# Optimization experiments

Hardware: AMD Instinct MI355X
Metric: run time of the kernel (lower is better)

The kernel has to match this reference:

```python
import jax, jax.numpy as jnp
import numpy as np
from jax import lax

K = 3      # kernel_size
C = 64     # n_feat
B, H, W = 2, 256, 256


def _conv(x, w, b, pad):
    # NCHW conv, stride 1
    out = lax.conv_general_dilated(x, w, (1, 1), [(pad, pad), (pad, pad)],
                                   dimension_numbers=('NCHW', 'OIHW', 'NCHW'))
    return out + b[None, :, None, None]


def _prelu(x, a):
    # nn.PReLU() with a single shared learnable slope (init 0.25)
    return jnp.where(x >= 0, x, a * x)


def setup_inputs():
    key = jax.random.key(0)
    ks = jax.random.split(key, 20)
    s = 0.05
    def w(k, shape):
        return jax.random.normal(k, shape, jnp.float32) * s
    inp = {
        'image': jax.random.normal(ks[0], (B, C, H, W), jnp.float32),
        'guidance': jax.random.normal(ks[1], (B, C, H, W), jnp.float32),
        # self.tensor: 1x1 conv (2C -> C) + PReLU (shared with jbf_conv's act)
        'tensor_w': w(ks[2], (C, 2 * C, 1, 1)),
        'tensor_b': jnp.zeros((C,), jnp.float32),
        'a_jbf': jnp.full((1,), 0.25, jnp.float32),
        'kg_w1': w(ks[3], (C, C, 3, 3)), 'kg_b1': jnp.zeros((C,), jnp.float32),
        'kg_w2': w(ks[4], (C, C, 3, 3)), 'kg_b2': jnp.zeros((C,), jnp.float32),
        'kg_w3': w(ks[5], (C, C, 3, 3)), 'kg_b3': jnp.zeros((C,), jnp.float32),
        'kg_w4': w(ks[6], (C, C, 3, 3)), 'kg_b4': jnp.zeros((C,), jnp.float32),
        'kg_w5': w(ks[7], (K * K * C, C, 1, 1)),
        'kg_b5': jnp.zeros((K * K * C,), jnp.float32),
        'a_kg': jnp.full((1,), 0.25, jnp.float32),
        # jbf_conv: 3x3 C->C, PReLU (shared a_jbf), 3x3 C->C
        'jbf_w1': w(ks[8], (C, C, 3, 3)), 'jbf_b1': jnp.zeros((C,), jnp.float32),
        'jbf_w2': w(ks[9], (C, C, 3, 3)), 'jbf_b2': jnp.zeros((C,), jnp.float32),
    }
    return inp


def reference(image, guidance, tensor_w, tensor_b, a_jbf,
              kg_w1, kg_b1, kg_w2, kg_b2, kg_w3, kg_b3, kg_w4, kg_b4,
              kg_w5, kg_b5, a_kg, jbf_w1, jbf_b1, jbf_w2, jbf_b2):
    b, c, h, w = image.shape
    # fuse target+guidance features
    t = _prelu(_conv(jnp.concatenate([image, guidance], axis=1), tensor_w, tensor_b, 0), a_jbf)
    # concat_kg: predict per-pixel dynamic kernel (b, K*K*c, h, w)
    y = t
    for wt, bs in ((kg_w1, kg_b1), (kg_w2, kg_b2), (kg_w3, kg_b3), (kg_w4, kg_b4)):
        y = _prelu(_conv(y, wt, bs, 1), a_kg)
    bi_kernel = _conv(y, kg_w5, kg_b5, 0)
    # unfold: torch layout is channel-major (c, ki, kj) along dim 1
    p = (K - 1) // 2
    xp = jnp.pad(image, ((0, 0), (0, 0), (p, p), (p, p)))
    taps = [xp[:, :, i:i + h, j:j + w] for i in range(K) for j in range(K)]
    patch = jnp.stack(taps, axis=2).reshape(b, c * K * K, h, w)
    # NOTE: faithful to source -- (c*K*K) flat layout reinterpreted as (K*K, c)
    jbf = (patch * bi_kernel).reshape(b, K * K, c, h, w).sum(axis=1)
    out = _conv(_prelu(_conv(jbf, jbf_w1, jbf_b1, 1), a_jbf), jbf_w2, jbf_b2, 1)
    return out + image
```

## Files before the change

kernel.cpp:

```cpp
#include <hip/hip_runtime.h>

#define HW 65536

typedef __bf16 bf16x8 __attribute__((ext_vector_type(8)));
typedef float f32x16 __attribute__((ext_vector_type(16)));

__device__ inline unsigned short f2bf(float x) {
    union { float f; unsigned u; } v; v.f = x;
    unsigned r = v.u + 0x7FFF + ((v.u >> 16) & 1);
    return (unsigned short)(r >> 16);
}
__device__ inline float bfhi2f(unsigned u) {
    union { unsigned u; float f; } v; v.u = u & 0xffff0000u; return v.f;
}
__device__ inline float bflo2f(unsigned u) {
    union { unsigned u; float f; } v; v.u = u << 16; return v.f;
}

union FragU { uint4 u; bf16x8 v; };
__device__ inline bf16x8 ld_frag(const uint4* p) { FragU t; t.u = *p; return t.v; }


__global__ __launch_bounds__(256) void k_wprep(
    const float* __restrict__ w0, const float* __restrict__ w1,
    const float* __restrict__ w2, const float* __restrict__ w3,
    const float* __restrict__ w4, const float* __restrict__ w5,
    const float* __restrict__ w5c, const float* __restrict__ tw,
    unsigned short* __restrict__ wT)
{
    int y = blockIdx.y;
    unsigned short* o = wT + (size_t)y * 36864;
    if (y < 6) {
        const float* ws_[6] = {w0, w1, w2, w3, w4, w5};
        const float* w = ws_[y];
        for (int e = blockIdx.x * 256 + threadIdx.x; e < 36864; e += gridDim.x * 256) {
            int tap = e >> 12, oc = (e >> 6) & 63, ic = e & 63;
            int igg = ic >> 3, j = ic & 7;
            int dst = ((tap * 8 + igg) * 64 + oc) * 8 + j;
            o[dst] = f2bf(w[(oc * 64 + ic) * 9 + tap]);
        }
    } else if (y == 6) {
        for (int e = blockIdx.x * 256 + threadIdx.x; e < 36864; e += gridDim.x * 256)
            o[e] = f2bf(w5c[e]);
    } else {
        for (int e = blockIdx.x * 256 + threadIdx.x; e < 8192; e += gridDim.x * 256) {
            int oc = e >> 7, ic = e & 127;
            int kg = ic >> 3, j = ic & 7;
            o[((kg * 64 + oc) << 3) + j] = f2bf(tw[e]);
        }
    }
}

__global__ __launch_bounds__(256) void k_tr(
    const float* __restrict__ img, const float* __restrict__ gd,
    unsigned short* __restrict__ imgT, unsigned short* __restrict__ gdT)
{
    __shared__ float sT[64 * 66];
    int tid = threadIdx.x;
    int z = blockIdx.y;
    int b = z & 1;
    const float* src = (z >> 1) ? gd : img;
    unsigned short* dst = (z >> 1) ? gdT : imgT;
    int px0 = blockIdx.x * 64;
    size_t sbase = (size_t)b * 64 * HW + px0;

#pragma unroll
    for (int i = 0; i < 4; ++i) {
        int e = i * 256 + tid;
        int ic = e >> 4, seg = e & 15;
        float4 v = *(const float4*)(src + sbase + (size_t)ic * HW + seg * 4);
        float* p = &sT[ic * 66 + seg * 4];
        ((float2*)p)[0] = make_float2(v.x, v.y);
        ((float2*)p)[1] = make_float2(v.z, v.w);
    }
    __syncthreads();

    size_t dbase = (size_t)b * HW * 64 + (size_t)px0 * 64;
#pragma unroll
    for (int k = 0; k < 2; ++k) {
        int idx = k * 256 + tid;
        int px = idx >> 3, u = idx & 7;
        union { uint4 q; unsigned short h[8]; } o;
#pragma unroll
        for (int j = 0; j < 8; ++j)
            o.h[j] = f2bf(sT[(u * 8 + j) * 66 + px]);
        *(uint4*)(dst + dbase + (size_t)px * 64 + u * 8) = o.q;
    }
}

__global__ __launch_bounds__(256, 4) void k_fusem(
    const unsigned short* __restrict__ imgT, const unsigned short* __restrict__ gdT,
    const unsigned short* __restrict__ wTf, const float* __restrict__ bias,
    const float* __restrict__ a, unsigned short* __restrict__ out)
{
    __shared__ __align__(16) char smem[18688];
    uint4* sX = (uint4*)smem;
    float* sB = (float*)(smem + 18432);
    unsigned short* sT16 = (unsigned short*)smem;

    int tid = threadIdx.x;
    int wv = tid >> 6, lane = tid & 63;
    int half = lane >> 5, l31 = lane & 31;
    int lin = blockIdx.x + (blockIdx.y << 4) + (blockIdx.z << 9);
    int slab = lin & 7, sub = lin >> 3;
    int b = slab >> 2;
    int y0 = (slab & 3) * 64 + (sub >> 4) * 8;
    int x0 = (sub & 15) * 16;
    size_t zbase = (size_t)b * HW * 64;
    const uint4* wg = (const uint4*)wTf;

    if (tid < 64) sB[tid] = bias[tid];

    f32x16 acc[2];
#pragma unroll
    for (int i = 0; i < 2; ++i)
#pragma unroll
        for (int r = 0; r < 16; ++r) acc[i][r] = 0.f;

    auto loadX = [&](const unsigned short* src, uint4* rx) {
#pragma unroll
        for (int i = 0; i < 4; ++i) {
            int e = i * 256 + tid;
            int px = e >> 3, ig = e & 7;
            int gy = y0 + (px >> 4), gx = x0 + (px & 15);
            rx[i] = *(const uint4*)(src + zbase + ((size_t)(gy * 256 + gx)) * 64 + ig * 8);
        }
    };
    auto writeX = [&](const uint4* rx) {
#pragma unroll
        for (int i = 0; i < 4; ++i) {
            int e = i * 256 + tid;
            sX[(e >> 3) * 9 + (e & 7)] = rx[i];
        }
    };
    auto compute = [&](int h) {
#pragma unroll
        for (int c = 0; c < 4; ++c) {
            int ig = c * 2 + half;
            int kg = h * 8 + ig;
            bf16x8 a0 = ld_frag(&wg[kg * 64 + l31]);
            bf16x8 a1 = ld_frag(&wg[kg * 64 + 32 + l31]);
            int p0 = wv * 32 + l31;
            bf16x8 b0 = ld_frag(&sX[p0 * 9 + ig]);
            acc[0] = __builtin_amdgcn_mfma_f32_32x32x16_bf16(a0, b0, acc[0], 0, 0, 0);
            acc[1] = __builtin_amdgcn_mfma_f32_32x32x16_bf16(a1, b0, acc[1], 0, 0, 0);
        }
    };

    uint4 rx[4], ry[4];
    loadX(imgT, rx);
    writeX(rx);
    loadX(gdT, ry);
    __syncthreads();
    compute(0);
    __syncthreads();
    writeX(ry);
    __syncthreads();
    compute(1);

    float slope = a[0];
    __syncthreads();
    {
        int px = wv * 32 + l31;
#pragma unroll
        for (int ot = 0; ot < 2; ++ot)
#pragma unroll
            for (int q2 = 0; q2 < 4; ++q2) {
                unsigned short hw[4];
#pragma unroll
                for (int j = 0; j < 4; ++j) {
                    int r = (q2 << 2) | j;
                    int oc = ot * 32 + j + 8 * q2 + 4 * half;
                    float v = acc[ot][r] + sB[oc];
                    v = (v >= 0.f) ? v : slope * v;
                    hw[j] = f2bf(v);
                }
                int unit = ot * 4 + q2;
                int up = unit ^ (px & 7);
                uint2* p = (uint2*)&sT16[px * 64 + up * 8 + half * 4];
                *p = make_uint2((unsigned)hw[0] | ((unsigned)hw[1] << 16),
                                (unsigned)hw[2] | ((unsigned)hw[3] << 16));
            }
    }
    __syncthreads();
#pragma unroll
    for (int k = 0; k < 4; ++k) {
        int idx = k * 256 + tid;
        int row = idx >> 7, rem = idx & 127;
        int col = rem >> 3, u = rem & 7;
        int px = row * 16 + col;
        uint4 v = *(uint4*)&sT16[px * 64 + (u ^ (px & 7)) * 8];
        *(uint4*)(out + zbase + ((size_t)((y0 + row) * 256 + x0 + col)) * 64 + u * 8) = v;
    }
}

#define XU 5

template<int MODE>
__global__ __launch_bounds__(256, 4) void k_conv2x(
    const unsigned short* __restrict__ in,
    const unsigned short* __restrict__ w1T, const unsigned short* __restrict__ w2T,
    const float* __restrict__ b1, const float* __restrict__ b2,
    const float* __restrict__ a, const float* __restrict__ res,
    void* __restrict__ outv)
{
    __shared__ __align__(16) char smem[38912];
    uint4* sIn0 = (uint4*)smem;
    uint4* sIn1 = (uint4*)(smem + 19200);
    float* sB = (float*)(smem + 38400);

    int tid = threadIdx.x;
    int wv = tid >> 6, lane = tid & 63;
    int half = lane >> 5, l31 = lane & 31;
    int w2 = wv >> 1, g = wv & 1;
    int lin = blockIdx.x + (blockIdx.y << 4) + (blockIdx.z << 9);
    int slab = lin & 7, sub = lin >> 3;
    int b = slab >> 2;
    int y0 = (slab & 3) * 64 + (sub >> 4) * 8;
    int x0 = (sub & 15) * 16;
    const size_t zbase = (size_t)b * HW * 64;
    const uint4* wg1 = (const uint4*)w1T;
    const uint4* wg2 = (const uint4*)w2T;

    if (tid < 64) sB[tid] = b1[tid];
    else if (tid < 128) sB[tid] = b2[tid - 64];

    auto loadIn = [&](int h, uint4* rx) {
#pragma unroll
        for (int i = 0; i < 4; ++i) {
            int e = i * 256 + tid;
            int cell = e >> 2, ig = e & 3;
            int r = cell / 20, c2 = cell - r * 20;
            int gy = y0 - 2 + r, gx = x0 - 2 + c2;
            rx[i] = make_uint4(0, 0, 0, 0);
            bool act = (i < 3) || (e < 960);
            if (act && gy >= 0 && gy < 256 && gx >= 0 && gx < 256)
                rx[i] = *(const uint4*)(in + zbase + ((size_t)(gy * 256 + gx)) * 64 + h * 32 + ig * 8);
        }
    };
    auto writeIn = [&](uint4* s, const uint4* rx) {
#pragma unroll
        for (int i = 0; i < 4; ++i) {
            int e = i * 256 + tid;
            if (i < 3 || e < 960) s[(e >> 2) * XU + (e & 3)] = rx[i];
        }
    };

    int cellv[3], ibv[3];
#pragma unroll
    for (int s = 0; s < 3; ++s) {
        int c = g * 96 + s * 32 + l31;
        cellv[s] = c;
        int cc = c < 180 ? c : 179;
        ibv[s] = (cc / 18) * 20 + (cc % 18);
    }

    f32x16 acc1[3];
#pragma unroll
    for (int s = 0; s < 3; ++s)
#pragma unroll
        for (int r = 0; r < 16; ++r) acc1[s][r] = 0.f;

    auto conv1_h = [&](int h, const uint4* sInp) {
#pragma unroll
        for (int dy = 0; dy < 3; ++dy) {
#pragma unroll
            for (int dx = 0; dx < 3; ++dx) {
                int tap = dy * 3 + dx;
                int doff = dy * 20 + dx;
#pragma unroll
                for (int c = 0; c < 2; ++c) {
                    int ig = c * 2 + half;
                    bf16x8 af = ld_frag(&wg1[(tap * 8 + h * 4 + ig) * 64 + w2 * 32 + l31]);
#pragma unroll
                    for (int s = 0; s < 3; ++s) {
                        bf16x8 bb = ld_frag(&sInp[(ibv[s] + doff) * XU + ig]);
                        acc1[s] = __builtin_amdgcn_mfma_f32_32x32x16_bf16(af, bb, acc1[s], 0, 0, 0);
                    }
                }
            }
        }
    };

    uint4 rx[4];
    loadIn(0, rx);
    writeIn(sIn0, rx);
    uint4 ry[4];
    loadIn(1, ry);
    __syncthreads();
    conv1_h(0, sIn0);
    writeIn(sIn1, ry);
    __syncthreads();
    conv1_h(1, sIn1);

    float s1 = a[0];
    __syncthreads();
    unsigned short* sC16 = (unsigned short*)smem;
#pragma unroll
    for (int s = 0; s < 3; ++s) {
        int cell = cellv[s];
        if (cell < 180) {
            int orow = cell / 18, ocol = cell - orow * 18;
            int gy = y0 - 1 + orow, gx = x0 - 1 + ocol;
            bool inb = (gy >= 0 && gy < 256 && gx >= 0 && gx < 256);
#pragma unroll
            for (int q2 = 0; q2 < 4; ++q2) {
                unsigned short hw[4];
#pragma unroll
                for (int j = 0; j < 4; ++j) {
                    int r = (q2 << 2) | j;
                    int oc = w2 * 32 + j + 8 * q2 + 4 * half;
                    float v = acc1[s][r] + sB[oc];
                    v = (v >= 0.f) ? v : s1 * v;
                    if (!inb) v = 0.f;
                    hw[j] = f2bf(v);
                }
                int up = (w2 * 4 + q2) ^ (cell & 7);
                *(uint2*)&sC16[cell * 64 + up * 8 + half * 4] =
                    make_uint2((unsigned)hw[0] | ((unsigned)hw[1] << 16),
                               (unsigned)hw[2] | ((unsigned)hw[3] << 16));
            }
        }
    }
    __syncthreads();

    f32x16 acc2[2];
#pragma unroll
    for (int s = 0; s < 2; ++s)
#pragma unroll
        for (int r = 0; r < 16; ++r) acc2[s][r] = 0.f;

    int rowS[2], colS[2];
#pragma unroll
    for (int s = 0; s < 2; ++s) {
        int px = g * 64 + s * 32 + l31;
        rowS[s] = px >> 4; colS[s] = px & 15;
    }
    {
        const uint4* sC4 = (const uint4*)smem;
#pragma unroll
        for (int dy = 0; dy < 3; ++dy) {
#pragma unroll
            for (int dx = 0; dx < 3; ++dx) {
                int tap = dy * 3 + dx;
#pragma unroll
                for (int c = 0; c < 4; ++c) {
                    int ig = c * 2 + half;
                    bf16x8 af = ld_frag(&wg2[(tap * 8 + ig) * 64 + w2 * 32 + l31]);
#pragma unroll
                    for (int s = 0; s < 2; ++s) {
                        int cl = (rowS[s] + dy) * 18 + colS[s] + dx;
                        bf16x8 bb = ld_frag(&sC4[cl * 8 + (ig ^ (cl & 7))]);
                        acc2[s] = __builtin_amdgcn_mfma_f32_32x32x16_bf16(af, bb, acc2[s], 0, 0, 0);
                    }
                }
            }
        }
    }

    if (MODE == 0) {
        __syncthreads();
        unsigned short* sT16 = (unsigned short*)smem;
#pragma unroll
        for (int s = 0; s < 2; ++s) {
            int px = g * 64 + s * 32 + l31;
#pragma unroll
            for (int q2 = 0; q2 < 4; ++q2) {
                unsigned short hw[4];
#pragma unroll
                for (int j = 0; j < 4; ++j) {
                    int r = (q2 << 2) | j;
                    int oc = w2 * 32 + j + 8 * q2 + 4 * half;
                    float v = acc2[s][r] + sB[64 + oc];
                    v = (v >= 0.f) ? v : s1 * v;
                    hw[j] = f2bf(v);
                }
                int up = (w2 * 4 + q2) ^ (px & 7);
                uint2* p = (uint2*)&sT16[px * 64 + up * 8 + half * 4];
                *p = make_uint2((unsigned)hw[0] | ((unsigned)hw[1] << 16),
                                (unsigned)hw[2] | ((unsigned)hw[3] << 16));
            }
        }
        __syncthreads();
        unsigned short* outT = (unsigned short*)outv;
#pragma unroll
        for (int k = 0; k < 4; ++k) {
            int idx = k * 256 + tid;
            int row = idx >> 7, rem = idx & 127;
            int col = rem >> 3, u = rem & 7;
            int px = row * 16 + col;
            uint4 v = *(uint4*)&sT16[px * 64 + (u ^ (px & 7)) * 8];
            *(uint4*)(outT + zbase + ((size_t)((y0 + row) * 256 + x0 + col)) * 64 + u * 8) = v;
        }
    } else {
        float* outF = (float*)outv;
#pragma unroll
        for (int s = 0; s < 2; ++s) {
            int px = g * 64 + s * 32 + l31;
            int y = y0 + (px >> 4), x = x0 + (px & 15);
            size_t pbase = (size_t)b * 64 * HW + (size_t)y * 256 + x;
#pragma unroll
            for (int r = 0; r < 16; ++r) {
                int oc = w2 * 32 + (r & 3) + 8 * (r >> 2) + 4 * half;
                float v = acc2[s][r] + sB[64 + oc];
                v += res[pbase + (size_t)oc * HW];
                outF[pbase + (size_t)oc * HW] = v;
            }
        }
    }
}

struct OffTab { unsigned v[9][32]; int chlo[9]; };
constexpr OffTab make_tab() {
    OffTab t{};
    for (int kk = 0; kk < 9; ++kk) {
        int chlo = (kk * 64) / 9;
        t.chlo[kk] = chlo;
        for (int ot = 0; ot < 2; ++ot)
            for (int r = 0; r < 16; ++r) {
                int cc0 = ot * 32 + (r & 3) + 8 * (r >> 2);
                int q0 = kk * 64 + cc0, q1 = q0 + 4;
                int o0 = (q0 / 9 - chlo) * 360 + (q0 % 9 / 3) * 40 + (q0 % 9 % 3);
                int o1 = (q1 / 9 - chlo) * 360 + (q1 % 9 / 3) * 40 + (q1 % 9 % 3);
                t.v[kk][ot * 16 + r] = (unsigned)o0 | ((unsigned)o1 << 16);
            }
    }
    return t;
}
__constant__ OffTab kOff = make_tab();

__global__ __launch_bounds__(256, 2) void k_jbfm(
    const unsigned short* __restrict__ y4, const float* __restrict__ img,
    const unsigned short* __restrict__ w5T, const float* __restrict__ b5,
    unsigned short* __restrict__ out)
{
    __shared__ __align__(16) char smem[78592];
    uint4* sY = (uint4*)smem;
    float* sB5 = (float*)(smem + 76288);
    unsigned short* sT16 = (unsigned short*)smem;

    int tid = threadIdx.x;
    int wv = tid >> 6, lane = tid & 63;
    int half = lane >> 5, l31 = lane & 31;
    int lin = blockIdx.x + (blockIdx.y << 3) + (blockIdx.z << 8);
    int slab = lin & 7, sub = lin >> 3;
    int b = slab >> 2;
    int y0 = (slab & 3) * 64 + (sub >> 3) * 8;
    int x0 = (sub & 7) * 32;
    size_t zbase = (size_t)b * HW * 64;
    size_t ibase = (size_t)b * 64 * HW;

    int p_off[3], p_dst[3];
    bool p_a[3], p_b[3], p_act[3];
#pragma unroll
    for (int i = 0; i < 3; ++i) {
        int e = i * 256 + tid;
        bool act = e < 720;
        int ch = e / 90, rem = e - ch * 90;
        int rp = rem / 10, seg = rem - rp * 10;
        int gy = y0 + rp - 1;
        int gxb = x0 - 4 + seg * 4;
        bool xok = (gxb >= 0 && gxb < 256);
        p_act[i] = act;
        p_a[i] = act && xok && gy >= 0 && gy < 256;
        p_b[i] = act && xok && (gy + 1) < 256;
        p_off[i] = ch * HW + gy * 256 + gxb;
        p_dst[i] = ch * 360 + rp * 40 + seg * 4;
    }

#pragma unroll
    for (int i = 0; i < 8; ++i) {
        int e = i * 256 + tid;
        int px = e >> 3, ig = e & 7;
        int gy = y0 + (px >> 5), gx = x0 + (px & 31);
        sY[px * 9 + ig] = *(const uint4*)(y4 + zbase + ((size_t)(gy * 256 + gx)) * 64 + ig * 8);
    }
    for (int e = tid; e < 576; e += 256) sB5[e] = b5[e];

    {
        uint4* sW50 = (uint4*)(smem + 36864);
        unsigned* sP0 = (unsigned*)(smem + 53248);
#pragma unroll
        for (int u = 0; u < 2; ++u) {
            int uu = u * 256 + tid;
            int cc = uu & 63, ig = uu >> 6;
            sW50[uu] = ((const uint4*)w5T)[cc * 8 + ig];
        }
        const float* rp0 = img + ibase;
#pragma unroll
        for (int i = 0; i < 3; ++i) {
            float4 fa = make_float4(0, 0, 0, 0), fb = make_float4(0, 0, 0, 0);
            if (p_a[i]) fa = *(const float4*)(rp0 + p_off[i]);
            if (p_b[i]) fb = *(const float4*)(rp0 + p_off[i] + 256);
            if (p_act[i]) {
                uint4 pk;
                pk.x = (unsigned)f2bf(fa.x) | ((unsigned)f2bf(fb.x) << 16);
                pk.y = (unsigned)f2bf(fa.y) | ((unsigned)f2bf(fb.y) << 16);
                pk.z = (unsigned)f2bf(fa.z) | ((unsigned)f2bf(fb.z) << 16);
                pk.w = (unsigned)f2bf(fa.w) | ((unsigned)f2bf(fb.w) << 16);
                *(uint4*)&sP0[p_dst[i]] = pk;
            }
        }
    }

    float jb[2][2][16];
#pragma unroll
    for (int i = 0; i < 2; ++i)
#pragma unroll
        for (int j = 0; j < 2; ++j)
#pragma unroll
            for (int r = 0; r < 16; ++r) jb[i][j][r] = 0.f;

    __syncthreads();

#pragma unroll 1
    for (int kk = 0; kk < 9; ++kk) {
        const int cur = kk & 1;
        const uint4* sW5c = (const uint4*)(smem + 36864 + cur * 8192);
        const unsigned* sPc = (const unsigned*)(smem + 53248 + cur * 11520);

        uint4 wpre0, wpre1;
        float4 pfa[3], pfb[3];
        if (kk < 8) {
            const int nk = kk + 1;
            const int chlo_n = kOff.chlo[nk];
            {
                int cc = tid & 63, ig = tid >> 6;
                wpre0 = ((const uint4*)w5T)[(nk * 64 + cc) * 8 + ig];
                int uu = 256 + tid;
                int cc1 = uu & 63, ig1 = uu >> 6;
                wpre1 = ((const uint4*)w5T)[(nk * 64 + cc1) * 8 + ig1];
            }
            const float* rp0 = img + ibase + (size_t)chlo_n * HW;
#pragma unroll
            for (int i = 0; i < 3; ++i) {
                pfa[i] = make_float4(0, 0, 0, 0);
                pfb[i] = make_float4(0, 0, 0, 0);
                if (p_a[i]) pfa[i] = *(const float4*)(rp0 + p_off[i]);
                if (p_b[i]) pfb[i] = *(const float4*)(rp0 + p_off[i] + 256);
            }
        }

        f32x16 acc[2][2];
#pragma unroll
        for (int ot = 0; ot < 2; ++ot)
#pragma unroll
            for (int r = 0; r < 16; ++r) {
                int cc0 = ot * 32 + (r & 3) + 8 * (r >> 2);
                float bv = sB5[kk * 64 + cc0 + 4 * half];
                acc[ot][0][r] = bv;
                acc[ot][1][r] = bv;
            }

#pragma unroll
        for (int c = 0; c < 4; ++c) {
            int ig = c * 2 + half;
            bf16x8 a0 = ld_frag(&sW5c[ig * 64 + l31]);
            bf16x8 a1 = ld_frag(&sW5c[ig * 64 + 32 + l31]);
            int p0 = wv * 64 + l31;
            bf16x8 b0 = ld_frag(&sY[p0 * 9 + ig]);
            bf16x8 b1 = ld_frag(&sY[(p0 + 32) * 9 + ig]);
            acc[0][0] = __builtin_amdgcn_mfma_f32_32x32x16_bf16(a0, b0, acc[0][0], 0, 0, 0);
            acc[0][1] = __builtin_amdgcn_mfma_f32_32x32x16_bf16(a0, b1, acc[0][1], 0, 0, 0);
            acc[1][0] = __builtin_amdgcn_mfma_f32_32x32x16_bf16(a1, b0, acc[1][0], 0, 0, 0);
            acc[1][1] = __builtin_amdgcn_mfma_f32_32x32x16_bf16(a1, b1, acc[1][1], 0, 0, 0);
        }

        {
            const unsigned* basep = sPc + wv * 80 + l31 + 3;
            const unsigned* tab = kOff.v[kk];
#pragma unroll
            for (int ot = 0; ot < 2; ++ot)
#pragma unroll
                for (int r = 0; r < 16; ++r) {
                    unsigned oo = tab[ot * 16 + r];
                    unsigned o0 = oo & 0xffffu, o1 = oo >> 16;
                    unsigned pv = basep[half ? o1 : o0];
                    jb[ot][0][r] = fmaf(acc[ot][0][r], bflo2f(pv), jb[ot][0][r]);
                    jb[ot][1][r] = fmaf(acc[ot][1][r], bfhi2f(pv), jb[ot][1][r]);
                }
        }

        if (kk < 8) {
            uint4* sW5n = (uint4*)(smem + 36864 + (cur ^ 1) * 8192);
            unsigned* sPn = (unsigned*)(smem + 53248 + (cur ^ 1) * 11520);
            sW5n[tid] = wpre0;
            sW5n[256 + tid] = wpre1;
#pragma unroll
            for (int i = 0; i < 3; ++i) {
                if (p_act[i]) {
                    uint4 pk;
                    pk.x = (unsigned)f2bf(pfa[i].x) | ((unsigned)f2bf(pfb[i].x) << 16);
                    pk.y = (unsigned)f2bf(pfa[i].y) | ((unsigned)f2bf(pfb[i].y) << 16);
                    pk.z = (unsigned)f2bf(pfa[i].z) | ((unsigned)f2bf(pfb[i].z) << 16);
                    pk.w = (unsigned)f2bf(pfa[i].w) | ((unsigned)f2bf(pfb[i].w) << 16);
                    *(uint4*)&sPn[p_dst[i]] = pk;
                }
            }
        }
        __syncthreads();
    }

#pragma unroll
    for (int ot = 0; ot < 2; ++ot)
#pragma unroll
        for (int pt = 0; pt < 2; ++pt) {
            int px = wv * 64 + pt * 32 + l31;
#pragma unroll
            for (int q2 = 0; q2 < 4; ++q2) {
                unsigned short hw[4];
#pragma unroll
                for (int j = 0; j < 4; ++j) {
                    int r = (q2 << 2) | j;
                    hw[j] = f2bf(jb[ot][pt][r]);
                }
                int unit = ot * 4 + q2;
                int up = unit ^ (px & 7);
                uint2* p = (uint2*)&sT16[px * 64 + up * 8 + half * 4];
                *p = make_uint2((unsigned)hw[0] | ((unsigned)hw[1] << 16),
                                (unsigned)hw[2] | ((unsigned)hw[3] << 16));
            }
        }
    __syncthreads();
#pragma unroll
    for (int k = 0; k < 8; ++k) {
        int col = tid >> 3, u = tid & 7;
        int px = k * 32 + col;
        uint4 v = *(uint4*)&sT16[px * 64 + (u ^ (px & 7)) * 8];
        *(uint4*)(out + zbase + ((size_t)((y0 + k) * 256 + x0 + col)) * 64 + u * 8) = v;
    }
}

extern "C" void kernel_launch(void* const* d_in, const int* in_sizes, int n_in,
                              void* d_out, int out_size, void* d_ws, size_t ws_size,
                              hipStream_t stream) {
    const float* img  = (const float*)d_in[0];
    const float* gd   = (const float*)d_in[1];
    const float* tw   = (const float*)d_in[2];
    const float* tb   = (const float*)d_in[3];
    const float* ajbf = (const float*)d_in[4];
    const float* kw1  = (const float*)d_in[5];
    const float* kb1  = (const float*)d_in[6];
    const float* kw2  = (const float*)d_in[7];
    const float* kb2  = (const float*)d_in[8];
    const float* kw3  = (const float*)d_in[9];
    const float* kb3  = (const float*)d_in[10];
    const float* kw4  = (const float*)d_in[11];
    const float* kb4  = (const float*)d_in[12];
    const float* kw5  = (const float*)d_in[13];
    const float* kb5  = (const float*)d_in[14];
    const float* akg  = (const float*)d_in[15];
    const float* jw1  = (const float*)d_in[16];
    const float* jb1  = (const float*)d_in[17];
    const float* jw2  = (const float*)d_in[18];
    const float* jb2  = (const float*)d_in[19];
    float* out  = (float*)d_out;

    const size_t TEN = (size_t)2 * HW * 64;
    unsigned short* bufA = (unsigned short*)d_ws;
    unsigned short* imgT = bufA + TEN;
    unsigned short* gdT  = imgT + TEN;
    unsigned short* wT   = gdT + TEN;
    unsigned short* bufB = (unsigned short*)d_out;
    unsigned short* bufC = gdT;

    dim3 gs(16, 32, 2);
    dim3 gw(8, 32, 2);

    k_tr<<<dim3(1024, 4), 256, 0, stream>>>(img, gd, imgT, gdT);
    k_wprep<<<dim3(4, 8), 256, 0, stream>>>(kw1, kw2, kw3, kw4, jw1, jw2, kw5, tw, wT);

    k_fusem<<<gs, 256, 0, stream>>>(imgT, gdT, wT + (size_t)7 * 36864, tb, ajbf, bufA);

    k_conv2x<0><<<gs, 256, 0, stream>>>(bufA, wT + (size_t)0 * 36864, wT + (size_t)1 * 36864,
                                        kb1, kb2, akg, nullptr, bufB);
    k_conv2x<0><<<gs, 256, 0, stream>>>(bufB, wT + (size_t)2 * 36864, wT + (size_t)3 * 36864,
                                        kb3, kb4, akg, nullptr, bufA);

    k_jbfm<<<gw, 256, 0, stream>>>(bufA, img, wT + (size_t)6 * 36864, kb5, bufC);

    k_conv2x<2><<<gs, 256, 0, stream>>>(bufC, wT + (size_t)4 * 36864, wT + (size_t)5 * 36864,
                                        jb1, jb2, ajbf, img, out);
}
```

Before: 303.1 us.

## Fuse 1x1 fusion conv with first two 3x3 convs; merge prep kernels

The transpose and weight-prep kernels are merged into a single launch. The 1x1 fuse conv is folded into the same kernel as the first two 3x3 kernel-generator convs. That kernel computes the 1x1 output over a tile with a 2-pixel halo, then runs both 3x3 convs from LDS with halo recompute, so the intermediate tensors no longer round-trip through global memory. It uses more LDS (about 54KB, down to 2 blocks per CU) and adds redundant halo computation.

```diff
diff --git a/kernel.cpp b/kernel.cpp
--- a/kernel.cpp
+++ b/kernel.cpp
@@ -21,166 +21,320 @@
 __device__ inline bf16x8 ld_frag(const uint4* p) { FragU t; t.u = *p; return t.v; }
 
 
-__global__ __launch_bounds__(256) void k_wprep(
+__global__ __launch_bounds__(256) void k_pre(
+    const float* __restrict__ img, const float* __restrict__ gd,
     const float* __restrict__ w0, const float* __restrict__ w1,
     const float* __restrict__ w2, const float* __restrict__ w3,
     const float* __restrict__ w4, const float* __restrict__ w5,
     const float* __restrict__ w5c, const float* __restrict__ tw,
+    unsigned short* __restrict__ imgT, unsigned short* __restrict__ gdT,
     unsigned short* __restrict__ wT)
-{
-    int y = blockIdx.y;
-    unsigned short* o = wT + (size_t)y * 36864;
-    if (y < 6) {
-        const float* ws_[6] = {w0, w1, w2, w3, w4, w5};
-        const float* w = ws_[y];
-        for (int e = blockIdx.x * 256 + threadIdx.x; e < 36864; e += gridDim.x * 256) {
-            int tap = e >> 12, oc = (e >> 6) & 63, ic = e & 63;
-            int igg = ic >> 3, j = ic & 7;
-            int dst = ((tap * 8 + igg) * 64 + oc) * 8 + j;
-            o[dst] = f2bf(w[(oc * 64 + ic) * 9 + tap]);
-        }
-    } else if (y == 6) {
-        for (int e = blockIdx.x * 256 + threadIdx.x; e < 36864; e += gridDim.x * 256)
-            o[e] = f2bf(w5c[e]);
-    } else {
-        for (int e = blockIdx.x * 256 + threadIdx.x; e < 8192; e += gridDim.x * 256) {
-            int oc = e >> 7, ic = e & 127;
-            int kg = ic >> 3, j = ic & 7;
-            o[((kg * 64 + oc) << 3) + j] = f2bf(tw[e]);
-        }
-    }
-}
-
-__global__ __launch_bounds__(256) void k_tr(
-    const float* __restrict__ img, const float* __restrict__ gd,
-    unsigned short* __restrict__ imgT, unsigned short* __restrict__ gdT)
 {
     __shared__ float sT[64 * 66];
     int tid = threadIdx.x;
-    int z = blockIdx.y;
-    int b = z & 1;
-    const float* src = (z >> 1) ? gd : img;
-    unsigned short* dst = (z >> 1) ? gdT : imgT;
-    int px0 = blockIdx.x * 64;
-    size_t sbase = (size_t)b * 64 * HW + px0;
-
-#pragma unroll
-    for (int i = 0; i < 4; ++i) {
-        int e = i * 256 + tid;
-        int ic = e >> 4, seg = e & 15;
-        float4 v = *(const float4*)(src + sbase + (size_t)ic * HW + seg * 4);
-        float* p = &sT[ic * 66 + seg * 4];
-        ((float2*)p)[0] = make_float2(v.x, v.y);
-        ((float2*)p)[1] = make_float2(v.z, v.w);
-    }
-    __syncthreads();
-
-    size_t dbase = (size_t)b * HW * 64 + (size_t)px0 * 64;
-#pragma unroll
-    for (int k = 0; k < 2; ++k) {
-        int idx = k * 256 + tid;
-        int px = idx >> 3, u = idx & 7;
-        union { uint4 q; unsigned short h[8]; } o;
-#pragma unroll
-        for (int j = 0; j < 8; ++j)
-            o.h[j] = f2bf(sT[(u * 8 + j) * 66 + px]);
-        *(uint4*)(dst + dbase + (size_t)px * 64 + u * 8) = o.q;
+    int y = blockIdx.y;
+    if (y < 4) {
+        int z = y;
+        int b = z & 1;
+        const float* src = (z >> 1) ? gd : img;
+        unsigned short* dst = (z >> 1) ? gdT : imgT;
+        int px0 = blockIdx.x * 64;
+        size_t sbase = (size_t)b * 64 * HW + px0;
+
+#pragma unroll
+        for (int i = 0; i < 4; ++i) {
+            int e = i * 256 + tid;
+            int ic = e >> 4, seg = e & 15;
+            float4 v = *(const float4*)(src + sbase + (size_t)ic * HW + seg * 4);
+            float* p = &sT[ic * 66 + seg * 4];
+            ((float2*)p)[0] = make_float2(v.x, v.y);
+            ((float2*)p)[1] = make_float2(v.z, v.w);
+        }
+        __syncthreads();
+
+        size_t dbase = (size_t)b * HW * 64 + (size_t)px0 * 64;
+#pragma unroll
+        for (int k = 0; k < 2; ++k) {
+            int idx = k * 256 + tid;
+            int px = idx >> 3, u = idx & 7;
+            union { uint4 q; unsigned short h[8]; } o;
+#pragma unroll
+            for (int j = 0; j < 8; ++j)
+                o.h[j] = f2bf(sT[(u * 8 + j) * 66 + px]);
+            *(uint4*)(dst + dbase + (size_t)px * 64 + u * 8) = o.q;
+        }
+    } else {
+        int y2 = y - 4;
+        unsigned short* o = wT + (size_t)y2 * 36864;
+        int e = blockIdx.x * 256 + tid;
+        if (y2 < 6) {
+            const float* ws_[6] = {w0, w1, w2, w3, w4, w5};
+            const float* w = ws_[y2];
+            if (e < 36864) {
+                int tap = e >> 12, oc = (e >> 6) & 63, ic = e & 63;
+                int igg = ic >> 3, j = ic & 7;
+                int dst = ((tap * 8 + igg) * 64 + oc) * 8 + j;
+                o[dst] = f2bf(w[(oc * 64 + ic) * 9 + tap]);
+            }
+        } else if (y2 == 6) {
+            if (e < 36864) o[e] = f2bf(w5c[e]);
+        } else {
+            if (e < 8192) {
+                int oc = e >> 7, ic = e & 127;
+                int kg = ic >> 3, j = ic & 7;
+                o[((kg * 64 + oc) << 3) + j] = f2bf(tw[e]);
+            }
+        }
     }
 }
 
-__global__ __launch_bounds__(256, 4) void k_fusem(
+__global__ __launch_bounds__(256, 2) void k_fuse3(
     const unsigned short* __restrict__ imgT, const unsigned short* __restrict__ gdT,
-    const unsigned short* __restrict__ wTf, const float* __restrict__ bias,
-    const float* __restrict__ a, unsigned short* __restrict__ out)
+    const unsigned short* __restrict__ wTf,
+    const unsigned short* __restrict__ w1T, const unsigned short* __restrict__ w2T,
+    const float* __restrict__ tb, const float* __restrict__ b1,
+    const float* __restrict__ b2, const float* __restrict__ ajbf,
+    const float* __restrict__ akg, unsigned short* __restrict__ out)
 {
-    __shared__ __align__(16) char smem[18688];
-    uint4* sX = (uint4*)smem;
-    float* sB = (float*)(smem + 18432);
-    unsigned short* sT16 = (unsigned short*)smem;
+    __shared__ __align__(16) char smem[54528];
+    float* sB = (float*)(smem + 53760);
+    uint4* sS0 = (uint4*)smem;
+    uint4* sS1 = (uint4*)(smem + 19200);
 
     int tid = threadIdx.x;
     int wv = tid >> 6, lane = tid & 63;
     int half = lane >> 5, l31 = lane & 31;
+    int w2 = wv >> 1, g = wv & 1;
     int lin = blockIdx.x + (blockIdx.y << 4) + (blockIdx.z << 9);
     int slab = lin & 7, sub = lin >> 3;
     int b = slab >> 2;
     int y0 = (slab & 3) * 64 + (sub >> 4) * 8;
     int x0 = (sub & 15) * 16;
-    size_t zbase = (size_t)b * HW * 64;
-    const uint4* wg = (const uint4*)wTf;
-
-    if (tid < 64) sB[tid] = bias[tid];
-
-    f32x16 acc[2];
-#pragma unroll
-    for (int i = 0; i < 2; ++i)
-#pragma unroll
-        for (int r = 0; r < 16; ++r) acc[i][r] = 0.f;
-
-    auto loadX = [&](const unsigned short* src, uint4* rx) {
+    const size_t zbase = (size_t)b * HW * 64;
+    const uint4* wgf = (const uint4*)wTf;
+    const uint4* wg1 = (const uint4*)w1T;
+    const uint4* wg2 = (const uint4*)w2T;
+
+    if (tid < 64) sB[tid] = tb[tid];
+    else if (tid < 128) sB[tid] = b1[tid - 64];
+    else if (tid < 192) sB[tid] = b2[tid - 128];
+
+    auto loadS = [&](int t, int h, uint4* rx) {
+        const unsigned short* src = t ? gdT : imgT;
 #pragma unroll
         for (int i = 0; i < 4; ++i) {
             int e = i * 256 + tid;
-            int px = e >> 3, ig = e & 7;
-            int gy = y0 + (px >> 4), gx = x0 + (px & 15);
-            rx[i] = *(const uint4*)(src + zbase + ((size_t)(gy * 256 + gx)) * 64 + ig * 8);
+            int cell = e >> 2, ig = e & 3;
+            int r = cell / 20, c2 = cell - r * 20;
+            int gy = y0 - 2 + r, gx = x0 - 2 + c2;
+            rx[i] = make_uint4(0, 0, 0, 0);
+            if (e < 960 && gy >= 0 && gy < 256 && gx >= 0 && gx < 256)
+                rx[i] = *(const uint4*)(src + zbase + ((size_t)(gy * 256 + gx)) * 64 + h * 32 + ig * 8);
         }
     };
-    auto writeX = [&](const uint4* rx) {
+    auto writeS = [&](uint4* s, const uint4* rx) {
 #pragma unroll
         for (int i = 0; i < 4; ++i) {
             int e = i * 256 + tid;
-            sX[(e >> 3) * 9 + (e & 7)] = rx[i];
+            if (e < 960) s[(e >> 2) * 5 + (e & 3)] = rx[i];
         }
     };
-    auto compute = [&](int h) {
-#pragma unroll
-        for (int c = 0; c < 4; ++c) {
+
+    int cell0[4];
+#pragma unroll
+    for (int s = 0; s < 4; ++s) {
+        int c = g * 128 + s * 32 + l31;
+        cell0[s] = c < 240 ? c : 239;
+    }
+    f32x16 acc0[4];
+#pragma unroll
+    for (int s = 0; s < 4; ++s)
+#pragma unroll
+        for (int r = 0; r < 16; ++r) acc0[s][r] = 0.f;
+
+    auto mm1 = [&](int t, int h, const uint4* sS) {
+#pragma unroll
+        for (int c = 0; c < 2; ++c) {
             int ig = c * 2 + half;
-            int kg = h * 8 + ig;
-            bf16x8 a0 = ld_frag(&wg[kg * 64 + l31]);
-            bf16x8 a1 = ld_frag(&wg[kg * 64 + 32 + l31]);
-            int p0 = wv * 32 + l31;
-            bf16x8 b0 = ld_frag(&sX[p0 * 9 + ig]);
-            acc[0] = __builtin_amdgcn_mfma_f32_32x32x16_bf16(a0, b0, acc[0], 0, 0, 0);
-            acc[1] = __builtin_amdgcn_mfma_f32_32x32x16_bf16(a1, b0, acc[1], 0, 0, 0);
+            int kg = t * 8 + h * 4 + ig;
+            bf16x8 af = ld_frag(&wgf[kg * 64 + w2 * 32 + l31]);
+#pragma unroll
+            for (int s = 0; s < 4; ++s) {
+                bf16x8 bb = ld_frag(&sS[cell0[s] * 5 + ig]);
+                acc0[s] = __builtin_amdgcn_mfma_f32_32x32x16_bf16(af, bb, acc0[s], 0, 0, 0);
+            }
         }
     };
 
-    uint4 rx[4], ry[4];
-    loadX(imgT, rx);
-    writeX(rx);
-    loadX(gdT, ry);
-    __syncthreads();
-    compute(0);
-    __syncthreads();
-    writeX(ry);
-    __syncthreads();
-    compute(1);
-
-    float slope = a[0];
-    __syncthreads();
-    {
-        int px = wv * 32 + l31;
-#pragma unroll
-        for (int ot = 0; ot < 2; ++ot)
+    uint4 rx[4];
+    loadS(0, 0, rx);
+    writeS(sS0, rx);
+    loadS(0, 1, rx);
+    __syncthreads();
+    mm1(0, 0, sS0);
+    writeS(sS1, rx);
+    loadS(1, 0, rx);
+    __syncthreads();
+    mm1(0, 1, sS1);
+    writeS(sS0, rx);
+    loadS(1, 1, rx);
+    __syncthreads();
+    mm1(1, 0, sS0);
+    writeS(sS1, rx);
+    __syncthreads();
+    mm1(1, 1, sS1);
+
+    float s_jbf = ajbf[0], s_kg = akg[0];
+    __syncthreads();
+    unsigned short* sC0 = (unsigned short*)smem;
+#pragma unroll
+    for (int s = 0; s < 4; ++s) {
+        int cell = g * 128 + s * 32 + l31;
+        if (cell < 240) {
+            int R = cell / 20, C = cell - R * 20;
+            int gy = y0 - 2 + R, gx = x0 - 2 + C;
+            bool inb = (gy >= 0 && gy < 256 && gx >= 0 && gx < 256);
 #pragma unroll
             for (int q2 = 0; q2 < 4; ++q2) {
                 unsigned short hw[4];
 #pragma unroll
                 for (int j = 0; j < 4; ++j) {
                     int r = (q2 << 2) | j;
-                    int oc = ot * 32 + j + 8 * q2 + 4 * half;
-                    float v = acc[ot][r] + sB[oc];
-                    v = (v >= 0.f) ? v : slope * v;
+                    int oc = w2 * 32 + j + 8 * q2 + 4 * half;
+                    float v = acc0[s][r] + sB[oc];
+                    v = (v >= 0.f) ? v : s_jbf * v;
+                    if (!inb) v = 0.f;
                     hw[j] = f2bf(v);
                 }
-                int unit = ot * 4 + q2;
-                int up = unit ^ (px & 7);
-                uint2* p = (uint2*)&sT16[px * 64 + up * 8 + half * 4];
-                *p = make_uint2((unsigned)hw[0] | ((unsigned)hw[1] << 16),
-                                (unsigned)hw[2] | ((unsigned)hw[3] << 16));
-            }
+                int up = (w2 * 4 + q2) ^ (cell & 7);
+                *(uint2*)&sC0[cell * 64 + up * 8 + half * 4] =
+                    make_uint2((unsigned)hw[0] | ((unsigned)hw[1] << 16),
+                               (unsigned)hw[2] | ((unsigned)hw[3] << 16));
+            }
+        }
+    }
+    __syncthreads();
+
+    int cellv[3], ibv[3];
+#pragma unroll
+    for (int s = 0; s < 3; ++s) {
+        int c = g * 96 + s * 32 + l31;
+        cellv[s] = c;
+        int cc = c < 180 ? c : 179;
+        ibv[s] = (cc / 18) * 20 + (cc % 18);
+    }
+    f32x16 acc1[3];
+#pragma unroll
+    for (int s = 0; s < 3; ++s)
+#pragma unroll
+        for (int r = 0; r < 16; ++r) acc1[s][r] = 0.f;
+
+    {
+        const uint4* sC04 = (const uint4*)smem;
+#pragma unroll
+        for (int dy = 0; dy < 3; ++dy) {
+#pragma unroll
+            for (int dx = 0; dx < 3; ++dx) {
+                int tap = dy * 3 + dx;
+                int doff = dy * 20 + dx;
+#pragma unroll
+                for (int c4 = 0; c4 < 4; ++c4) {
+                    int unit = c4 * 2 + half;
+                    bf16x8 af = ld_frag(&wg1[(tap * 8 + unit) * 64 + w2 * 32 + l31]);
+#pragma unroll
+                    for (int s = 0; s < 3; ++s) {
+                        int cc = ibv[s] + doff;
+                        bf16x8 bb = ld_frag(&sC04[cc * 8 + (unit ^ (cc & 7))]);
+                        acc1[s] = __builtin_amdgcn_mfma_f32_32x32x16_bf16(af, bb, acc1[s], 0, 0, 0);
+                    }
+                }
+            }
+        }
+    }
+
+    unsigned short* sC1 = (unsigned short*)(smem + 30720);
+#pragma unroll
+    for (int s = 0; s < 3; ++s) {
+        int cell = cellv[s];
+        if (cell < 180) {
+            int orow = cell / 18, ocol = cell - orow * 18;
+            int gy = y0 - 1 + orow, gx = x0 - 1 + ocol;
+            bool inb = (gy >= 0 && gy < 256 && gx >= 0 && gx < 256);
+#pragma unroll
+            for (int q2 = 0; q2 < 4; ++q2) {
+                unsigned short hw[4];
+#pragma unroll
+                for (int j = 0; j < 4; ++j) {
+                    int r = (q2 << 2) | j;
+                    int oc = w2 * 32 + j + 8 * q2 + 4 * half;
+                    float v = acc1[s][r] + sB[64 + oc];
+                    v = (v >= 0.f) ? v : s_kg * v;
+                    if (!inb) v = 0.f;
+                    hw[j] = f2bf(v);
+                }
+                int up = (w2 * 4 + q2) ^ (cell & 7);
+                *(uint2*)&sC1[cell * 64 + up * 8 + half * 4] =
+                    make_uint2((unsigned)hw[0] | ((unsigned)hw[1] << 16),
+                               (unsigned)hw[2] | ((unsigned)hw[3] << 16));
+            }
+        }
+    }
+    __syncthreads();
+
+    f32x16 acc2[2];
+#pragma unroll
+    for (int s = 0; s < 2; ++s)
+#pragma unroll
+        for (int r = 0; r < 16; ++r) acc2[s][r] = 0.f;
+
+    int rowS[2], colS[2];
+#pragma unroll
+    for (int s = 0; s < 2; ++s) {
+        int px = g * 64 + s * 32 + l31;
+        rowS[s] = px >> 4; colS[s] = px & 15;
+    }
+    {
+        const uint4* sC14 = (const uint4*)(smem + 30720);
+#pragma unroll
+        for (int dy = 0; dy < 3; ++dy) {
+#pragma unroll
+            for (int dx = 0; dx < 3; ++dx) {
+                int tap = dy * 3 + dx;
+#pragma unroll
+                for (int c = 0; c < 4; ++c) {
+                    int ig = c * 2 + half;
+                    bf16x8 af = ld_frag(&wg2[(tap * 8 + ig) * 64 + w2 * 32 + l31]);
+#pragma unroll
+                    for (int s = 0; s < 2; ++s) {
+                        int cl = (rowS[s] + dy) * 18 + colS[s] + dx;
+                        bf16x8 bb = ld_frag(&sC14[cl * 8 + (ig ^ (cl & 7))]);
+                        acc2[s] = __builtin_amdgcn_mfma_f32_32x32x16_bf16(af, bb, acc2[s], 0, 0, 0);
+                    }
+                }
+            }
+        }
+    }
+
+    unsigned short* sT16 = (unsigned short*)smem;
+#pragma unroll
+    for (int s = 0; s < 2; ++s) {
+        int px = g * 64 + s * 32 + l31;
+#pragma unroll
+        for (int q2 = 0; q2 < 4; ++q2) {
+            unsigned short hw[4];
+#pragma unroll
+            for (int j = 0; j < 4; ++j) {
+                int r = (q2 << 2) | j;
+                int oc = w2 * 32 + j + 8 * q2 + 4 * half;
+                float v = acc2[s][r] + sB[128 + oc];
+                v = (v >= 0.f) ? v : s_kg * v;
+                hw[j] = f2bf(v);
+            }
+            int up = (w2 * 4 + q2) ^ (px & 7);
+            uint2* p = (uint2*)&sT16[px * 64 + up * 8 + half * 4];
+            *p = make_uint2((unsigned)hw[0] | ((unsigned)hw[1] << 16),
+                            (unsigned)hw[2] | ((unsigned)hw[3] << 16));
+        }
     }
     __syncthreads();
 #pragma unroll
@@ -667,17 +821,17 @@
     dim3 gs(16, 32, 2);
     dim3 gw(8, 32, 2);
 
-    k_tr<<<dim3(1024, 4), 256, 0, stream>>>(img, gd, imgT, gdT);
-    k_wprep<<<dim3(4, 8), 256, 0, stream>>>(kw1, kw2, kw3, kw4, jw1, jw2, kw5, tw, wT);
-
-    k_fusem<<<gs, 256, 0, stream>>>(imgT, gdT, wT + (size_t)7 * 36864, tb, ajbf, bufA);
-
-    k_conv2x<0><<<gs, 256, 0, stream>>>(bufA, wT + (size_t)0 * 36864, wT + (size_t)1 * 36864,
-                                        kb1, kb2, akg, nullptr, bufB);
-    k_conv2x<0><<<gs, 256, 0, stream>>>(bufB, wT + (size_t)2 * 36864, wT + (size_t)3 * 36864,
-                                        kb3, kb4, akg, nullptr, bufA);
-
-    k_jbfm<<<gw, 256, 0, stream>>>(bufA, img, wT + (size_t)6 * 36864, kb5, bufC);
+    k_pre<<<dim3(1024, 12), 256, 0, stream>>>(img, gd, kw1, kw2, kw3, kw4,
+                                              jw1, jw2, kw5, tw, imgT, gdT, wT);
+
+    k_fuse3<<<gs, 256, 0, stream>>>(imgT, gdT, wT + (size_t)7 * 36864,
+                                    wT + (size_t)0 * 36864, wT + (size_t)1 * 36864,
+                                    tb, kb1, kb2, ajbf, akg, bufA);
+
+    k_conv2x<0><<<gs, 256, 0, stream>>>(bufA, wT + (size_t)2 * 36864, wT + (size_t)3 * 36864,
+                                        kb3, kb4, akg, nullptr, bufB);
+
+    k_jbfm<<<gw, 256, 0, stream>>>(bufB, img, wT + (size_t)6 * 36864, kb5, bufC);
 
     k_conv2x<2><<<gs, 256, 0, stream>>>(bufC, wT + (size_t)4 * 36864, wT + (size_t)5 * 36864,
                                         jb1, jb2, ajbf, img, out);
```

After: 288.9 us. 1.05x faster.
